# Optimization experiments

Measured on AMD Instinct MI355X. Metric: run time of the kernel, lower is better.

## Reference

```python
import jax, jax.numpy as jnp
import numpy as np

N, C = 4194304, 10
EPS = 1e-10
FOCAL_EPS = 1e-8
TEMP, THETA = 0.01, 0.1
NUM_TH = 21


def setup_inputs() -> dict:
    key = jax.random.key(0)
    k1, k2 = jax.random.split(key)
    logits = jax.random.normal(k1, (N, C), dtype=jnp.float32)
    probs = jax.nn.softmax(logits, axis=1)
    labels = jax.random.randint(k2, (N,), 0, C)
    y = jax.nn.one_hot(labels, C, dtype=jnp.float32)
    return {"probs": probs, "y": y}


def _soft_T(e):
    # sigmoid( (1/temp) * log( e*(1-theta) / clamp((1-e)*theta, eps) ) )
    num = e * (1.0 - THETA)
    den = jnp.maximum((1.0 - e) * THETA, EPS)
    frac = jnp.maximum(num / den, EPS)
    return jax.nn.sigmoid(jnp.log(frac) / TEMP)


def reference(probs, y):
    entmax = jnp.log(jnp.asarray(C, dtype=probs.dtype))
    predictions = jnp.argmax(probs, axis=1)             # [N]
    labels = jnp.argmax(y)                              # scalar (flattened argmax, as in torch code)

    # predictive uncertainty (type=0): entropy of probs per-sample
    unc = -jnp.sum(probs * jnp.log(jnp.maximum(probs, EPS)), axis=1)  # [N]

    th_list = jnp.linspace(0.0, 1.0, NUM_TH, dtype=probs.dtype)       # [21]
    umin, umax = jnp.min(unc), jnp.max(unc)
    unc_th = umin + th_list * (umax - umin)                           # [21]

    s = _soft_T(unc / entmax)                                         # [N]
    t = jnp.tanh(unc)                                                 # [N]
    w_cert = (1.0 - s) * (1.0 - t)   # weight when counted as 'certain'
    w_unc = s * t                    # weight when counted as 'uncertain'

    acc = (predictions == labels).astype(probs.dtype)                 # [N]
    inacc = 1.0 - acc

    le = (unc[None, :] <= unc_th[:, None]).astype(probs.dtype)        # [21, N]
    gt = 1.0 - le

    # one parallel masked-reduction pass over all 21 thresholds
    n_ac = le @ (acc * w_cert)
    n_au = gt @ (acc * w_unc)
    n_ic = le @ (inacc * w_cert)
    n_iu = gt @ (inacc * w_unc)

    avu = (n_ac + n_iu) / (n_ac + n_au + n_ic + n_iu + EPS)           # [21]

    # trapezoid rule over increasing th_list (direction = +1)
    dx = jnp.diff(th_list)
    auc_avu = jnp.sum((avu[1:] + avu[:-1]) * 0.5 * dx)

    # FocalLoss(gamma=1)
    logp = jnp.log(jnp.maximum(probs, FOCAL_EPS))
    ce_per = -jnp.sum(y * logp, axis=1)
    focal_per = -jnp.sum(y * logp * (1.0 - probs), axis=1)
    focal_loss = jnp.mean(focal_per)
    ce_loss = jnp.mean(ce_per)

    beta = 1.0
    savu_loss = -beta * jnp.log(jnp.maximum(auc_avu, EPS)) + focal_loss
    return (savu_loss, ce_loss)
```

## Files before the change

### kernel.cpp

```cpp
#include <hip/hip_runtime.h>

#define C 10
#define CHUNK_ROWS 128
#define CHUNK_FLOATS 1280

__device__ __forceinline__ float waveSum(float v) {
#pragma unroll
  for (int o = 32; o > 0; o >>= 1) v += __shfl_down(v, o, 64);
  return v;
}
__device__ __forceinline__ float waveMin(float v) {
#pragma unroll
  for (int o = 32; o > 0; o >>= 1) v = fminf(v, __shfl_down(v, o, 64));
  return v;
}
__device__ __forceinline__ float waveMax(float v) {
#pragma unroll
  for (int o = 32; o > 0; o >>= 1) v = fmaxf(v, __shfl_down(v, o, 64));
  return v;
}
__device__ __forceinline__ unsigned waveMaxU(unsigned v) {
#pragma unroll
  for (int o = 32; o > 0; o >>= 1) {
    unsigned w = (unsigned)__shfl_down((int)v, o, 64);
    v = v > w ? v : w;
  }
  return v;
}

#define GLD16(gp, lp)                                             \
  __builtin_amdgcn_global_load_lds(                               \
      (__attribute__((address_space(1))) void*)(gp),              \
      (__attribute__((address_space(3))) void*)(lp), 16, 0, 0)

__global__ __launch_bounds__(256, 4) void pass1(
    const float* __restrict__ probs, const float* __restrict__ y,
    float2* __restrict__ us2,
    unsigned* __restrict__ uminInvSlots, unsigned* __restrict__ umaxSlots,
    float* __restrict__ ceSlots, float* __restrict__ focalSlots,
    int nchunks) {
  __shared__ float lds[4 * 2 * CHUNK_FLOATS];
  const int tid = threadIdx.x;
  const int widx = tid >> 6, lane = tid & 63;
  float* const wbuf = lds + widx * (2 * CHUNK_FLOATS);

  const int gw = blockIdx.x * 4 + widx;
  const int NW = gridDim.x * 4;

  int label0 = 0;
  {
    float m = y[0];
#pragma unroll
    for (int c = 1; c < C; ++c) {
      float v = y[c];
      if (v > m) { m = v; label0 = c; }
    }
  }

  const float4* y4 = (const float4*)y;

  auto issueP = [&](int c, int b) {
    const float* gp = probs + (size_t)c * CHUNK_FLOATS + (size_t)lane * 4;
    float* lp = wbuf + b * CHUNK_FLOATS + lane * 4;
#pragma unroll
    for (int q = 0; q < 5; ++q) GLD16(gp + q * 256, lp + q * 256);
  };
  auto issueY = [&](int c, float4* Yr) {
    const float4* gy = y4 + (size_t)c * 320 + lane;
#pragma unroll
    for (int q = 0; q < 5; ++q) Yr[q] = gy[q * 64];
  };

  float ceA = 0.f, foA = 0.f;
  float mnA = __uint_as_float(0x7f800000u), mxA = 0.f;
  float4 Ycur[5], Ynxt[5];

  if (gw < nchunks) { issueP(gw, 0); issueY(gw, Ycur); }
  int b = 0;
  for (int c = gw; c < nchunks; c += NW, b ^= 1) {
    if (c + NW < nchunks) { issueP(c + NW, b ^ 1); issueY(c + NW, Ynxt); }
    const float4* buff4 = (const float4*)(wbuf + b * CHUNK_FLOATS);

#pragma unroll
    for (int q = 0; q < 5; ++q) {
      float4 pv = buff4[q * 64 + lane];
      float4 yv = Ycur[q];
      float lpx = __logf(fmaxf(pv.x, 1e-8f));
      float lpy = __logf(fmaxf(pv.y, 1e-8f));
      float lpz = __logf(fmaxf(pv.z, 1e-8f));
      float lpw = __logf(fmaxf(pv.w, 1e-8f));
      float tx = yv.x * lpx, ty = yv.y * lpy, tz = yv.z * lpz, tw = yv.w * lpw;
      ceA -= tx + ty + tz + tw;
      foA -= tx * (1.f - pv.x) + ty * (1.f - pv.y) + tz * (1.f - pv.z) + tw * (1.f - pv.w);
    }

    float P[20];
#pragma unroll
    for (int q = 0; q < 5; ++q) {
      float4 v = buff4[lane * 5 + q];
      P[4 * q] = v.x; P[4 * q + 1] = v.y; P[4 * q + 2] = v.z; P[4 * q + 3] = v.w;
    }
    int am0 = 0, am1 = 0;
    float m0 = P[0], m1 = P[10];
#pragma unroll
    for (int cc = 1; cc < C; ++cc) {
      if (P[cc] > m0) { m0 = P[cc]; am0 = cc; }
      if (P[10 + cc] > m1) { m1 = P[10 + cc]; am1 = cc; }
    }
    float u0 = 0.f, u1 = 0.f;
#pragma unroll
    for (int cc = 0; cc < C; ++cc) {
      u0 -= P[cc] * __logf(fmaxf(P[cc], 1e-10f));
      u1 -= P[10 + cc] * __logf(fmaxf(P[10 + cc], 1e-10f));
    }
    mnA = fminf(mnA, fminf(u0, u1));
    mxA = fmaxf(mxA, fmaxf(u0, u1));

    unsigned s0 = __float_as_uint(u0) | ((am0 == label0) ? 0u : 0x80000000u);
    unsigned s1 = __float_as_uint(u1) | ((am1 == label0) ? 0u : 0x80000000u);
    us2[(size_t)c * 64 + lane] = make_float2(__uint_as_float(s0), __uint_as_float(s1));

#pragma unroll
    for (int q = 0; q < 5; ++q) Ycur[q] = Ynxt[q];
  }

  float ce = waveSum(ceA), fo = waveSum(foA);
  float mn = waveMin(mnA), mx = waveMax(mxA);
  if (lane == 0) {
    int slot = gw & 63;
    atomicAdd(&ceSlots[slot], ce);
    atomicAdd(&focalSlots[slot], fo);
    atomicMax(&uminInvSlots[slot], ~__float_as_uint(mn));
    atomicMax(&umaxSlots[slot], __float_as_uint(mx));
  }
}

__global__ __launch_bounds__(256, 4) void pass2(
    const float4* __restrict__ us4, int n4,
    const unsigned* __restrict__ uminInvSlots, const unsigned* __restrict__ umaxSlots,
    float* __restrict__ ghist) {
  __shared__ float hist[88 * 64];
  __shared__ float smm[2];
  const int tid = threadIdx.x, lane = tid & 63;
  for (int i = tid; i < 88 * 64; i += 256) hist[i] = 0.f;
  if (tid < 64) {
    unsigned mnInv = waveMaxU(uminInvSlots[tid]);
    unsigned mxb = waveMaxU(umaxSlots[tid]);
    if (tid == 0) { smm[0] = __uint_as_float(~mnInv); smm[1] = __uint_as_float(mxb); }
  }
  __syncthreads();
  const float umin = smm[0], delta = smm[1] - smm[0];
  float th[21];
#pragma unroll
  for (int k = 0; k < 21; ++k) th[k] = fmaf(0.05f * (float)k, delta, umin);

  const int stride = gridDim.x * 256;
  for (int i = blockIdx.x * 256 + tid; i < n4; i += stride) {
    float4 v = us4[i];
    float vv[4] = {v.x, v.y, v.z, v.w};
#pragma unroll
    for (int q = 0; q < 4; ++q) {
      unsigned b = __float_as_uint(vv[q]);
      int rb = (b >> 31) ? 44 : 0;
      float u = __uint_as_float(b & 0x7fffffffu);
      float e = u * 0.4342944819f;
      float lnum = __logf(e * 0.9f);
      float lden = __logf(fmaxf((1.f - e) * 0.1f, 1e-10f));
      float x = fmaxf(lnum - lden, -23.0258509f) * 100.f;
      float s = __builtin_amdgcn_rcpf(1.f + __expf(-x));
      float t = 1.f - 2.f * __builtin_amdgcn_rcpf(__expf(2.f * u) + 1.f);
      float wc = (1.f - s) * (1.f - t), wu = s * t;
      int j = 0;
#pragma unroll
      for (int k = 0; k < 21; ++k) j += (u > th[k]) ? 1 : 0;
      atomicAdd(&hist[(rb + j) * 64 + lane], wc);
      atomicAdd(&hist[(rb + 22 + j) * 64 + lane], wu);
    }
  }
  __syncthreads();
#pragma unroll
  for (int st = 32; st >= 1; st >>= 1) {
    for (int idx = tid; idx < 88 * st; idx += 256) {
      int r = idx / st, c = idx - r * st;
      hist[r * 64 + c] += hist[r * 64 + c + st];
    }
    __syncthreads();
  }
  int slot = blockIdx.x & 63;
  for (int r = tid; r < 88; r += 256)
    atomicAdd(&ghist[slot * 88 + r], hist[r * 64]);
}

__global__ __launch_bounds__(256) void pass3(
    const float* __restrict__ ghist,
    const float* __restrict__ ceSlots, const float* __restrict__ focalSlots,
    float* __restrict__ out, float invN) {
  __shared__ float hr[88];
  __shared__ float scf[2];
  int tid = threadIdx.x;
  if (tid < 88) {
    float s = 0.f;
    for (int q = 0; q < 64; ++q) s += ghist[q * 88 + tid];
    hr[tid] = s;
  }
  if (tid >= 128 && tid < 192) {
    int l = tid - 128;
    float ce = waveSum(ceSlots[l]);
    float fo = waveSum(focalSlots[l]);
    if (l == 0) { scf[0] = ce; scf[1] = fo; }
  }
  __syncthreads();
  if (tid == 0) {
    float H0[22], H1[22], H2[22], H3[22];
    float totAU = 0.f, totIU = 0.f;
    for (int j = 0; j < 22; ++j) {
      H0[j] = hr[j]; H1[j] = hr[22 + j]; H2[j] = hr[44 + j]; H3[j] = hr[66 + j];
      totAU += H1[j]; totIU += H3[j];
    }
    float n_ac = 0.f, n_ic = 0.f, n_au = totAU, n_iu = totIU;
    float auc = 0.f, prev = 0.f;
    for (int k = 0; k < 21; ++k) {
      n_ac += H0[k]; n_ic += H2[k];
      n_au -= H1[k]; n_iu -= H3[k];
      float avu = (n_ac + n_iu) / (n_ac + n_au + n_ic + n_iu + 1e-10f);
      if (k > 0) auc += (avu + prev) * 0.5f * 0.05f;
      prev = avu;
    }
    out[0] = -logf(fmaxf(auc, 1e-10f)) + scf[1] * invN;
    out[1] = scf[0] * invN;
  }
}

extern "C" void kernel_launch(void* const* d_in, const int* in_sizes, int n_in,
                              void* d_out, int out_size, void* d_ws, size_t ws_size,
                              hipStream_t stream) {
  const float* probs = (const float*)d_in[0];
  const float* y = (const float*)d_in[1];
  float* out = (float*)d_out;
  const int N = in_sizes[0] / C;

  float* wsf = (float*)d_ws;
  unsigned* uminInvSlots = (unsigned*)wsf;
  unsigned* umaxSlots = (unsigned*)(wsf + 64);
  float* ceSlots = wsf + 128;
  float* focalSlots = wsf + 192;
  float* ghist = wsf + 256;
  float* us = wsf + 5888;

  hipMemsetAsync(d_ws, 0, 5888 * sizeof(float), stream);

  const int nchunks = N / CHUNK_ROWS;
  pass1<<<1024, 256, 0, stream>>>(probs, y, (float2*)us, uminInvSlots, umaxSlots,
                                  ceSlots, focalSlots, nchunks);
  pass2<<<1024, 256, 0, stream>>>((const float4*)us, N / 4, uminInvSlots, umaxSlots,
                                  ghist);
  pass3<<<1, 256, 0, stream>>>(ghist, ceSlots, focalSlots, out, 1.0f / (float)N);
}
```

Measured before the change: 399.9 us.

## Load probs via registers and reuse one log for entropy and focal terms

Replaces the async global-to-LDS double-buffered load of probs with register float4 loads, prefetching the next chunk after the current one has been staged into LDS. The per-element log is now computed once in the coalesced layout and reused: p*log(p) is written to LDS for the row-wise entropy, and the focal/CE log is clamped to log(1e-8). This removes the 20 duplicate logs per lane in the transposed phase. Blocks shrink to 128 threads with twice as many blocks. The cost is extra LDS traffic for the second buffer and less overlap, since loads are now synchronous register loads with only one chunk in flight.

```diff
diff --git a/kernel.cpp b/kernel.cpp
--- a/kernel.cpp
+++ b/kernel.cpp
@@ -3,6 +3,7 @@
 #define C 10
 #define CHUNK_ROWS 128
 #define CHUNK_FLOATS 1280
+#define CHUNK_F4 320
 
 __device__ __forceinline__ float waveSum(float v) {
 #pragma unroll
@@ -28,100 +29,90 @@
   return v;
 }
 
-#define GLD16(gp, lp)                                             \
-  __builtin_amdgcn_global_load_lds(                               \
-      (__attribute__((address_space(1))) void*)(gp),              \
-      (__attribute__((address_space(3))) void*)(lp), 16, 0, 0)
-
-__global__ __launch_bounds__(256, 4) void pass1(
-    const float* __restrict__ probs, const float* __restrict__ y,
+__global__ __launch_bounds__(128, 4) void pass1(
+    const float4* __restrict__ probs4, const float4* __restrict__ y4,
     float2* __restrict__ us2,
     unsigned* __restrict__ uminInvSlots, unsigned* __restrict__ umaxSlots,
     float* __restrict__ ceSlots, float* __restrict__ focalSlots,
     int nchunks) {
-  __shared__ float lds[4 * 2 * CHUNK_FLOATS];
-  const int tid = threadIdx.x;
-  const int widx = tid >> 6, lane = tid & 63;
-  float* const wbuf = lds + widx * (2 * CHUNK_FLOATS);
-
-  const int gw = blockIdx.x * 4 + widx;
-  const int NW = gridDim.x * 4;
+  __shared__ float lds[2 * 2 * CHUNK_FLOATS];
+  const int widx = threadIdx.x >> 6, lane = threadIdx.x & 63;
+  float4* const bufP = (float4*)(lds + widx * (2 * CHUNK_FLOATS));
+  float4* const bufS = bufP + CHUNK_F4;
+
+  const int gw = blockIdx.x * 2 + widx;
+  const int NW = gridDim.x * 2;
 
   int label0 = 0;
   {
-    float m = y[0];
+    const float* yf = (const float*)y4;
+    float m = yf[0];
 #pragma unroll
     for (int c = 1; c < C; ++c) {
-      float v = y[c];
+      float v = yf[c];
       if (v > m) { m = v; label0 = c; }
     }
   }
 
-  const float4* y4 = (const float4*)y;
-
-  auto issueP = [&](int c, int b) {
-    const float* gp = probs + (size_t)c * CHUNK_FLOATS + (size_t)lane * 4;
-    float* lp = wbuf + b * CHUNK_FLOATS + lane * 4;
-#pragma unroll
-    for (int q = 0; q < 5; ++q) GLD16(gp + q * 256, lp + q * 256);
-  };
-  auto issueY = [&](int c, float4* Yr) {
-    const float4* gy = y4 + (size_t)c * 320 + lane;
-#pragma unroll
-    for (int q = 0; q < 5; ++q) Yr[q] = gy[q * 64];
+  float4 P[5], Y[5];
+  auto issue = [&](int c) {
+    const float4* gp = probs4 + (size_t)c * CHUNK_F4 + lane;
+    const float4* gy = y4 + (size_t)c * CHUNK_F4 + lane;
+#pragma unroll
+    for (int q = 0; q < 5; ++q) { P[q] = gp[q * 64]; Y[q] = gy[q * 64]; }
   };
 
   float ceA = 0.f, foA = 0.f;
   float mnA = __uint_as_float(0x7f800000u), mxA = 0.f;
-  float4 Ycur[5], Ynxt[5];
-
-  if (gw < nchunks) { issueP(gw, 0); issueY(gw, Ycur); }
-  int b = 0;
-  for (int c = gw; c < nchunks; c += NW, b ^= 1) {
-    if (c + NW < nchunks) { issueP(c + NW, b ^ 1); issueY(c + NW, Ynxt); }
-    const float4* buff4 = (const float4*)(wbuf + b * CHUNK_FLOATS);
-
+
+  if (gw < nchunks) issue(gw);
+  for (int c = gw; c < nchunks; c += NW) {
 #pragma unroll
     for (int q = 0; q < 5; ++q) {
-      float4 pv = buff4[q * 64 + lane];
-      float4 yv = Ycur[q];
-      float lpx = __logf(fmaxf(pv.x, 1e-8f));
-      float lpy = __logf(fmaxf(pv.y, 1e-8f));
-      float lpz = __logf(fmaxf(pv.z, 1e-8f));
-      float lpw = __logf(fmaxf(pv.w, 1e-8f));
-      float tx = yv.x * lpx, ty = yv.y * lpy, tz = yv.z * lpz, tw = yv.w * lpw;
+      float4 pv = P[q], yv = Y[q];
+      float lpx = __logf(fmaxf(pv.x, 1e-10f));
+      float lpy = __logf(fmaxf(pv.y, 1e-10f));
+      float lpz = __logf(fmaxf(pv.z, 1e-10f));
+      float lpw = __logf(fmaxf(pv.w, 1e-10f));
+      float4 sv = make_float4(pv.x * lpx, pv.y * lpy, pv.z * lpz, pv.w * lpw);
+      float tx = yv.x * fmaxf(lpx, -18.420681f);
+      float ty = yv.y * fmaxf(lpy, -18.420681f);
+      float tz = yv.z * fmaxf(lpz, -18.420681f);
+      float tw = yv.w * fmaxf(lpw, -18.420681f);
       ceA -= tx + ty + tz + tw;
-      foA -= tx * (1.f - pv.x) + ty * (1.f - pv.y) + tz * (1.f - pv.z) + tw * (1.f - pv.w);
-    }
-
-    float P[20];
+      foA -= tx * (1.f - pv.x) + ty * (1.f - pv.y) + tz * (1.f - pv.z) +
+             tw * (1.f - pv.w);
+      bufP[q * 64 + lane] = pv;
+      bufS[q * 64 + lane] = sv;
+    }
+
+    if (c + NW < nchunks) issue(c + NW);
+
+    float R[20], S[20];
 #pragma unroll
     for (int q = 0; q < 5; ++q) {
-      float4 v = buff4[lane * 5 + q];
-      P[4 * q] = v.x; P[4 * q + 1] = v.y; P[4 * q + 2] = v.z; P[4 * q + 3] = v.w;
+      float4 v = bufP[lane * 5 + q];
+      R[4 * q] = v.x; R[4 * q + 1] = v.y; R[4 * q + 2] = v.z; R[4 * q + 3] = v.w;
+      float4 w = bufS[lane * 5 + q];
+      S[4 * q] = w.x; S[4 * q + 1] = w.y; S[4 * q + 2] = w.z; S[4 * q + 3] = w.w;
     }
     int am0 = 0, am1 = 0;
-    float m0 = P[0], m1 = P[10];
+    float m0 = R[0], m1 = R[10];
 #pragma unroll
     for (int cc = 1; cc < C; ++cc) {
-      if (P[cc] > m0) { m0 = P[cc]; am0 = cc; }
-      if (P[10 + cc] > m1) { m1 = P[10 + cc]; am1 = cc; }
-    }
-    float u0 = 0.f, u1 = 0.f;
-#pragma unroll
-    for (int cc = 0; cc < C; ++cc) {
-      u0 -= P[cc] * __logf(fmaxf(P[cc], 1e-10f));
-      u1 -= P[10 + cc] * __logf(fmaxf(P[10 + cc], 1e-10f));
-    }
+      if (R[cc] > m0) { m0 = R[cc]; am0 = cc; }
+      if (R[10 + cc] > m1) { m1 = R[10 + cc]; am1 = cc; }
+    }
+    float u0 = -(((S[0] + S[1]) + (S[2] + S[3])) + ((S[4] + S[5]) + (S[6] + S[7])) +
+                 (S[8] + S[9]));
+    float u1 = -(((S[10] + S[11]) + (S[12] + S[13])) +
+                 ((S[14] + S[15]) + (S[16] + S[17])) + (S[18] + S[19]));
     mnA = fminf(mnA, fminf(u0, u1));
     mxA = fmaxf(mxA, fmaxf(u0, u1));
 
     unsigned s0 = __float_as_uint(u0) | ((am0 == label0) ? 0u : 0x80000000u);
     unsigned s1 = __float_as_uint(u1) | ((am1 == label0) ? 0u : 0x80000000u);
     us2[(size_t)c * 64 + lane] = make_float2(__uint_as_float(s0), __uint_as_float(s1));
-
-#pragma unroll
-    for (int q = 0; q < 5; ++q) Ycur[q] = Ynxt[q];
   }
 
   float ce = waveSum(ceA), fo = waveSum(foA);
@@ -250,7 +241,8 @@
   hipMemsetAsync(d_ws, 0, 5888 * sizeof(float), stream);
 
   const int nchunks = N / CHUNK_ROWS;
-  pass1<<<1024, 256, 0, stream>>>(probs, y, (float2*)us, uminInvSlots, umaxSlots,
+  pass1<<<2048, 128, 0, stream>>>((const float4*)probs, (const float4*)y,
+                                  (float2*)us, uminInvSlots, umaxSlots,
                                   ceSlots, focalSlots, nchunks);
   pass2<<<1024, 256, 0, stream>>>((const float4*)us, N / 4, uminInvSlots, umaxSlots,
                                   ghist);
```

Measured after the change: 385.7 us. 1.04x faster.
